# Performance work log

Hardware: AMD Instinct MI355X
Metric: run time of the kernel (lower is better)

## Reference

```python
import jax, jax.numpy as jnp
import numpy as np

HEAD_DIM = 128

def setup_inputs() -> dict:
    key = jax.random.key(0)
    k1, k2, k3 = jax.random.split(key, 3)
    B, Q, H, D = 1, 2048, 32, HEAD_DIM
    KV = 2048
    q = jax.random.normal(k1, (B, Q, H, D), dtype=jnp.float32)
    k = jax.random.normal(k2, (B, KV, H, D), dtype=jnp.float32)
    v = jax.random.normal(k3, (B, KV, H, D), dtype=jnp.float32)
    return {"q": q, "k": k, "v": v}

def reference(q, k, v):
    B, Q, H, D = q.shape
    KV = k.shape[1]
    scale = 1.0 / jnp.sqrt(jnp.asarray(D, dtype=q.dtype))
    # [B,H,Q,KV] scores
    scores = jnp.einsum('bqhd,bkhd->bhqk', q, k) * scale
    # causal mask: disallow j > i + (KV - Q)
    i = jnp.arange(Q)[:, None]
    j = jnp.arange(KV)[None, :]
    causal = j <= i + (KV - Q)  # [Q,KV]
    scores = jnp.where(causal[None, None], scores, -jnp.inf)
    probs = jax.nn.softmax(scores.astype(jnp.float32), axis=-1)
    out = jnp.einsum('bhqk,bkhd->bqhd', probs.astype(q.dtype), v)
    roco_score = probs.sum(axis=2)            # [B,H,KV]
    roco_sq_score = (probs ** 2).sum(axis=2)  # [B,H,KV]
    return out, roco_score, roco_sq_score
```

## Files before the change

kernel.cpp:

```cpp
#include <hip/hip_runtime.h>
#include <hip/hip_bf16.h>

typedef unsigned short u16;
typedef __attribute__((ext_vector_type(8))) short bf16x8;
typedef __attribute__((ext_vector_type(4))) float f32x4;

#define NH   32
#define HD   128
#define SEQ  2048
#define BQ   64
#define BK   64

#define VT_OFF 8192

__device__ __forceinline__ int vt_key(int d) { return (d & 7) ^ ((d >> 3) & 7); }

__device__ __forceinline__ u16 f2b(float x) {
  __hip_bfloat16 hb = __float2bfloat16(x);
  return *(u16*)&hb;
}

__device__ __forceinline__ bf16x8 cvt8(const float* src) {
  float4 a = *(const float4*)(src);
  float4 b = *(const float4*)(src + 4);
  u16 t[8];
  t[0] = f2b(a.x); t[1] = f2b(a.y); t[2] = f2b(a.z); t[3] = f2b(a.w);
  t[4] = f2b(b.x); t[5] = f2b(b.y); t[6] = f2b(b.z); t[7] = f2b(b.w);
  return *(bf16x8*)t;
}

__device__ __forceinline__ bf16x8 cvt8s(const float* src, float sc) {
  float4 a = *(const float4*)(src);
  float4 b = *(const float4*)(src + 4);
  u16 t[8];
  t[0] = f2b(a.x * sc); t[1] = f2b(a.y * sc); t[2] = f2b(a.z * sc); t[3] = f2b(a.w * sc);
  t[4] = f2b(b.x * sc); t[5] = f2b(b.y * sc); t[6] = f2b(b.z * sc); t[7] = f2b(b.w * sc);
  return *(bf16x8*)t;
}

__device__ __forceinline__ void dma16(const u16* g, u16* l) {
  __builtin_amdgcn_global_load_lds(
      (const __attribute__((address_space(1))) void*)g,
      (__attribute__((address_space(3))) void*)l, 16, 0, 0);
}

__global__ __launch_bounds__(256)
void prep(const float* __restrict__ K, const float* __restrict__ V,
          u16* __restrict__ Kb, u16* __restrict__ Vtb) {
  __shared__ __align__(16) u16 T[64 * 136];
  int b = (int)blockIdx.x;
  int tid = (int)threadIdx.x;
  if (b < 4096) {
    size_t i = (size_t)b * 256 + tid;
    bf16x8 v = cvt8(K + i * 8);
    *(uint4*)(Kb + i * 8) = *(uint4*)&v;
  } else {
    b -= 4096;
    int h = b >> 5, jt = b & 31;
    #pragma unroll
    for (int it = 0; it < 4; ++it) {
      int c = tid + it * 256;
      int j = c >> 4, grp = c & 15;
      bf16x8 v = cvt8(V + ((size_t)(jt * 64 + j) * NH + h) * HD + (grp << 3));
      *(uint4*)(T + j * 136 + ((grp ^ ((j >> 3) & 7)) << 3)) = *(uint4*)&v;
    }
    __syncthreads();
    #pragma unroll
    for (int it = 0; it < 2; ++it) {
      int c = tid + it * 256;
      int d0 = (c >> 3) << 1, k = c & 7, jg = k << 3;
      int off = (((d0 >> 3) ^ k) << 3) | (d0 & 7);
      u16 lo[8], hi[8];
      #pragma unroll
      for (int e = 0; e < 8; ++e) {
        unsigned w = *(const unsigned*)(T + (jg + e) * 136 + off);
        lo[e] = (u16)w; hi[e] = (u16)(w >> 16);
      }
      *(uint4*)(Vtb + ((size_t)h * HD + d0) * SEQ + jt * 64 + jg) = *(uint4*)lo;
      *(uint4*)(Vtb + ((size_t)h * HD + d0 + 1) * SEQ + jt * 64 + jg) = *(uint4*)hi;
    }
  }
}

template <bool PRE>
__global__ __launch_bounds__(256)
void attn_roco(const float* __restrict__ Qg, const float* __restrict__ Kg,
               const float* __restrict__ Vg, const u16* __restrict__ Kb,
               const u16* __restrict__ Vtb, float* __restrict__ Og,
               float* __restrict__ RS) {
  __shared__ __align__(16) u16 smem[16384];
  u16* Ks = smem;
  u16* Vt = smem + VT_OFF;
  u16* Ps = smem;

  const int tid = threadIdx.x;
  const int wv  = tid >> 6;
  const int ln  = tid & 63;
  const int qd  = ln >> 4;
  const int cc  = ln & 15;

  const int h = (int)blockIdx.x & 31;
  const int pos = ((int)blockIdx.x >> 5) & 7;
  const int grp = (int)blockIdx.x >> 8;
  int qt;
  if      (grp == 0) qt = 31 - pos;
  else if (grp == 1) qt = 16 + pos;
  else if (grp == 2) qt = 15 - pos;
  else               qt = pos;

  const int qbase  = qt * BQ;
  const int ntiles = qt + 1;

  const float qsc = 0.08838834764831845f * 1.4426950408889634f;
  bf16x8 qf[4];
  {
    const float* qp = Qg + ((size_t)(qbase + wv * 16 + cc) * NH + h) * HD;
    #pragma unroll
    for (int kd = 0; kd < 4; ++kd)
      qf[kd] = cvt8s(qp + kd * 32 + qd * 8, qsc);
  }

  const int rbase = wv * 16 + qd * 4;
  float ls[4] = {0.f, 0.f, 0.f, 0.f};

  if (PRE) {
    const int ntA = (qt >> 1) + 1;
    for (int ta = 0; ta < ntA; ++ta) {
      __syncthreads();
      #pragma unroll
      for (int it = 0; it < 8; ++it) {
        int c = it * 256 + tid;
        int row = c >> 4, g = (c & 15) ^ (row & 15);
        dma16(Kb + ((size_t)(ta * 128 + row) * NH + h) * HD + (g << 3),
              smem + (size_t)c * 8);
      }
      __syncthreads();

      f32x4 S[8];
      #pragma unroll
      for (int f = 0; f < 8; ++f)
        #pragma unroll
        for (int r = 0; r < 4; ++r) S[f][r] = 0.f;

      #pragma unroll
      for (int kd = 0; kd < 4; ++kd) {
        #pragma unroll
        for (int f = 0; f < 8; ++f) {
          bf16x8 b = *(const bf16x8*)(smem + (f * 16 + cc) * 128 +
                                      (((kd * 4 + qd) ^ cc) << 3));
          S[f] = __builtin_amdgcn_mfma_f32_16x16x32_bf16(qf[kd], b, S[f], 0, 0, 0);
        }
      }

      const bool last = (ta == ntA - 1);
      #pragma unroll
      for (int r = 0; r < 4; ++r) {
        const int ig = qbase + rbase + r;
        float acc = 0.f;
        #pragma unroll
        for (int f = 0; f < 8; ++f) {
          float e = __builtin_amdgcn_exp2f(S[f][r]);
          if (last && (ta * 128 + f * 16 + cc) > ig) e = 0.f;
          acc += e;
        }
        ls[r] += acc;
      }
    }
  } else {
    for (int t = 0; t < ntiles; ++t) {
      __syncthreads();
      #pragma unroll
      for (int it = 0; it < 4; ++it) {
        int c = tid + it * 256;
        int row = c >> 4, g = c & 15;
        bf16x8 kv = cvt8(Kg + ((size_t)(t * BK + row) * NH + h) * HD + (g << 3));
        *(uint4*)(Ks + row * 128 + ((g ^ (row & 15)) << 3)) = *(uint4*)&kv;
      }
      __syncthreads();

      f32x4 S[4];
      #pragma unroll
      for (int f = 0; f < 4; ++f)
        #pragma unroll
        for (int r = 0; r < 4; ++r) S[f][r] = 0.f;

      #pragma unroll
      for (int kd = 0; kd < 4; ++kd) {
        #pragma unroll
        for (int f = 0; f < 4; ++f) {
          bf16x8 b = *(const bf16x8*)(Ks + (f * 16 + cc) * 128 +
                                      (((kd * 4 + qd) ^ cc) << 3));
          S[f] = __builtin_amdgcn_mfma_f32_16x16x32_bf16(qf[kd], b, S[f], 0, 0, 0);
        }
      }

      const bool diag = (t == qt);
      #pragma unroll
      for (int r = 0; r < 4; ++r) {
        const int iloc = rbase + r;
        float acc = 0.f;
        #pragma unroll
        for (int f = 0; f < 4; ++f) {
          float e = __builtin_amdgcn_exp2f(S[f][r]);
          if (diag && (f * 16 + cc) > iloc) e = 0.f;
          acc += e;
        }
        ls[r] += acc;
      }
    }
  }

  float invl[4];
  #pragma unroll
  for (int r = 0; r < 4; ++r) {
    #pragma unroll
    for (int off = 1; off < 16; off <<= 1)
      ls[r] += __shfl_xor(ls[r], off);
    invl[r] = 1.f / ls[r];
  }

  f32x4 O[8];
  #pragma unroll
  for (int f = 0; f < 8; ++f)
    #pragma unroll
    for (int r = 0; r < 4; ++r) O[f][r] = 0.f;

  float* ws_s = RS + (size_t)h * SEQ;
  float* ws_q = RS + (size_t)NH * SEQ + (size_t)h * SEQ;

  for (int t = 0; t < ntiles; ++t) {
    __syncthreads();
    if (PRE) {
      #pragma unroll
      for (int it = 0; it < 4; ++it) {
        int c = it * 256 + tid;
        int row = c >> 4, g = (c & 15) ^ (row & 15);
        dma16(Kb + ((size_t)(t * BK + row) * NH + h) * HD + (g << 3),
              Ks + (size_t)c * 8);
      }
      #pragma unroll
      for (int it = 0; it < 4; ++it) {
        int c = it * 256 + tid;
        int d = c >> 3, g = (c & 7) ^ vt_key(d);
        dma16(Vtb + ((size_t)h * HD + d) * SEQ + t * BK + (g << 3),
              Vt + (size_t)c * 8);
      }
    } else {
      #pragma unroll
      for (int it = 0; it < 4; ++it) {
        int c = tid + it * 256;
        int row = c >> 4, g = c & 15;
        bf16x8 kv = cvt8(Kg + ((size_t)(t * BK + row) * NH + h) * HD + (g << 3));
        *(uint4*)(Ks + row * 128 + ((g ^ (row & 15)) << 3)) = *(uint4*)&kv;
      }
      #pragma unroll
      for (int it = 0; it < 4; ++it) {
        int c = tid + it * 256;
        int j = c >> 4, d0 = (c & 15) << 3;
        bf16x8 v = cvt8(Vg + ((size_t)(t * BK + j) * NH + h) * HD + d0);
        u16 ev[8];
        *(uint4*)ev = *(uint4*)&v;
        #pragma unroll
        for (int e = 0; e < 8; ++e) {
          int d = d0 + e;
          Vt[d * BK + ((((j >> 3) ^ vt_key(d)) << 3)) + (j & 7)] = ev[e];
        }
      }
    }
    __syncthreads();

    f32x4 S[4];
    #pragma unroll
    for (int f = 0; f < 4; ++f)
      #pragma unroll
      for (int r = 0; r < 4; ++r) S[f][r] = 0.f;

    #pragma unroll
    for (int kd = 0; kd < 4; ++kd) {
      #pragma unroll
      for (int f = 0; f < 4; ++f) {
        bf16x8 b = *(const bf16x8*)(Ks + (f * 16 + cc) * 128 +
                                    (((kd * 4 + qd) ^ cc) << 3));
        S[f] = __builtin_amdgcn_mfma_f32_16x16x32_bf16(qf[kd], b, S[f], 0, 0, 0);
      }
    }

    __syncthreads();

    const bool diag = (t == qt);
    float cs[4] = {0.f, 0.f, 0.f, 0.f}, cq[4] = {0.f, 0.f, 0.f, 0.f};
    #pragma unroll
    for (int r = 0; r < 4; ++r) {
      const int iloc = rbase + r;
      const int prow = wv * 16 + qd * 4 + r;
      #pragma unroll
      for (int f = 0; f < 4; ++f) {
        float p = __builtin_amdgcn_exp2f(S[f][r]) * invl[r];
        if (diag && (f * 16 + cc) > iloc) p = 0.f;
        cs[f] += p;
        cq[f] += p * p;
        int pg = f * 2 + (cc >> 3);
        Ps[prow * 64 + ((pg ^ (prow & 7)) << 3) + (cc & 7)] = f2b(p);
      }
    }
    #pragma unroll
    for (int f = 0; f < 4; ++f) {
      cs[f] += __shfl_xor(cs[f], 16); cs[f] += __shfl_xor(cs[f], 32);
      cq[f] += __shfl_xor(cq[f], 16); cq[f] += __shfl_xor(cq[f], 32);
      if (qd == f) {
        int j = t * BK + f * 16 + cc;
        atomicAdd(ws_s + j, cs[f]);
        atomicAdd(ws_q + j, cq[f]);
      }
    }
    #pragma unroll
    for (int ks2 = 0; ks2 < 2; ++ks2) {
      bf16x8 a = *(const bf16x8*)(Ps + (wv * 16 + cc) * 64 +
                                  (((ks2 * 4 + qd) ^ (cc & 7)) << 3));
      #pragma unroll
      for (int f2 = 0; f2 < 8; ++f2) {
        int d = f2 * 16 + cc;
        int jb = ks2 * 4 + qd;
        bf16x8 b = *(const bf16x8*)(Vt + d * BK + ((jb ^ vt_key(d)) << 3));
        O[f2] = __builtin_amdgcn_mfma_f32_16x16x32_bf16(a, b, O[f2], 0, 0, 0);
      }
    }
  }

  #pragma unroll
  for (int f2 = 0; f2 < 8; ++f2) {
    #pragma unroll
    for (int r = 0; r < 4; ++r) {
      int i = qbase + rbase + r;
      int d = f2 * 16 + cc;
      Og[((size_t)i * NH + h) * HD + d] = O[f2][r];
    }
  }
}

extern "C" void kernel_launch(void* const* d_in, const int* in_sizes, int n_in,
                              void* d_out, int out_size, void* d_ws, size_t ws_size,
                              hipStream_t stream) {
  (void)in_sizes; (void)n_in; (void)out_size;
  const float* Qg = (const float*)d_in[0];
  const float* Kg = (const float*)d_in[1];
  const float* Vg = (const float*)d_in[2];
  float* Og = (float*)d_out;

  const size_t roco_elems = (size_t)2 * NH * SEQ;
  const size_t tens = (size_t)SEQ * NH * HD;
  const size_t need = 2 * tens * 2;
  const bool pre = ws_size >= need;

  float* RS = Og + tens;
  (void)hipMemsetAsync(RS, 0, roco_elems * sizeof(float), stream);

  u16* Kb  = (u16*)d_ws;
  u16* Vtb = Kb + tens;

  if (pre) {
    prep<<<dim3(4096 + 1024), dim3(256), 0, stream>>>(Kg, Vg, Kb, Vtb);
    attn_roco<true><<<dim3(NH * (SEQ / BQ)), dim3(256), 0, stream>>>(
        Qg, Kg, Vg, Kb, Vtb, Og, RS);
  } else {
    attn_roco<false><<<dim3(NH * (SEQ / BQ)), dim3(256), 0, stream>>>(
        Qg, Kg, Vg, Kb, Vtb, Og, RS);
  }
}
```

Before: 239.1 us.

## Transpose denominator pass to split keys across waves and skip masked key rows

```diff
diff --git a/kernel.cpp b/kernel.cpp
--- a/kernel.cpp
+++ b/kernel.cpp
@@ -12,6 +12,7 @@
 #define BK   64
 
 #define VT_OFF 8192
+#define PS_OFF 16384
 
 __device__ __forceinline__ int vt_key(int d) { return (d & 7) ^ ((d >> 3) & 7); }
 
@@ -88,10 +89,10 @@
                const float* __restrict__ Vg, const u16* __restrict__ Kb,
                const u16* __restrict__ Vtb, float* __restrict__ Og,
                float* __restrict__ RS) {
-  __shared__ __align__(16) u16 smem[16384];
+  __shared__ __align__(16) u16 smem[20480];
   u16* Ks = smem;
   u16* Vt = smem + VT_OFF;
-  u16* Ps = smem;
+  u16* Ps = smem + PS_OFF;
 
   const int tid = threadIdx.x;
   const int wv  = tid >> 6;
@@ -121,10 +122,20 @@
   }
 
   const int rbase = wv * 16 + qd * 4;
-  float ls[4] = {0.f, 0.f, 0.f, 0.f};
+  float invl[4];
 
   if (PRE) {
     const int ntA = (qt >> 1) + 1;
+    bf16x8 qa[4][4];
+    #pragma unroll
+    for (int fq = 0; fq < 4; ++fq) {
+      const float* qp = Qg + ((size_t)(qbase + fq * 16 + cc) * NH + h) * HD;
+      #pragma unroll
+      for (int kd = 0; kd < 4; ++kd)
+        qa[fq][kd] = cvt8s(qp + kd * 32 + qd * 8, qsc);
+    }
+    float lsw[4] = {0.f, 0.f, 0.f, 0.f};
+
     for (int ta = 0; ta < ntA; ++ta) {
       __syncthreads();
       #pragma unroll
@@ -136,37 +147,65 @@
       }
       __syncthreads();
 
-      f32x4 S[8];
-      #pragma unroll
-      for (int f = 0; f < 8; ++f)
-        #pragma unroll
-        for (int r = 0; r < 4; ++r) S[f][r] = 0.f;
-
-      #pragma unroll
-      for (int kd = 0; kd < 4; ++kd) {
-        #pragma unroll
-        for (int f = 0; f < 8; ++f) {
-          bf16x8 b = *(const bf16x8*)(smem + (f * 16 + cc) * 128 +
-                                      (((kd * 4 + qd) ^ cc) << 3));
-          S[f] = __builtin_amdgcn_mfma_f32_16x16x32_bf16(qf[kd], b, S[f], 0, 0, 0);
+      const bool last = (ta == ntA - 1);
+      const int rem = qbase + 64 - ta * 128;
+      if (!last || wv * 32 < rem) {
+        f32x4 S0[4], S1[4];
+        #pragma unroll
+        for (int fq = 0; fq < 4; ++fq)
+          #pragma unroll
+          for (int r = 0; r < 4; ++r) { S0[fq][r] = 0.f; S1[fq][r] = 0.f; }
+
+        #pragma unroll
+        for (int kd = 0; kd < 4; ++kd) {
+          bf16x8 a0 = *(const bf16x8*)(smem + (wv * 32 + cc) * 128 +
+                                       (((kd * 4 + qd) ^ cc) << 3));
+          bf16x8 a1 = *(const bf16x8*)(smem + (wv * 32 + 16 + cc) * 128 +
+                                       (((kd * 4 + qd) ^ cc) << 3));
+          #pragma unroll
+          for (int fq = 0; fq < 4; ++fq) {
+            S0[fq] = __builtin_amdgcn_mfma_f32_16x16x32_bf16(a0, qa[fq][kd], S0[fq], 0, 0, 0);
+            S1[fq] = __builtin_amdgcn_mfma_f32_16x16x32_bf16(a1, qa[fq][kd], S1[fq], 0, 0, 0);
+          }
         }
-      }
-
-      const bool last = (ta == ntA - 1);
-      #pragma unroll
-      for (int r = 0; r < 4; ++r) {
-        const int ig = qbase + rbase + r;
-        float acc = 0.f;
-        #pragma unroll
-        for (int f = 0; f < 8; ++f) {
-          float e = __builtin_amdgcn_exp2f(S[f][r]);
-          if (last && (ta * 128 + f * 16 + cc) > ig) e = 0.f;
-          acc += e;
+
+        const int kb = ta * 128 + wv * 32 + qd * 4;
+        #pragma unroll
+        for (int fq = 0; fq < 4; ++fq) {
+          const int qg = qbase + fq * 16 + cc;
+          float acc = 0.f;
+          #pragma unroll
+          for (int r = 0; r < 4; ++r) {
+            float e0 = __builtin_amdgcn_exp2f(S0[fq][r]);
+            float e1 = __builtin_amdgcn_exp2f(S1[fq][r]);
+            if (last && (kb + r) > qg) e0 = 0.f;
+            if (last && (kb + 16 + r) > qg) e1 = 0.f;
+            acc += e0 + e1;
+          }
+          lsw[fq] += acc;
         }
-        ls[r] += acc;
-      }
+      }
+    }
+    #pragma unroll
+    for (int fq = 0; fq < 4; ++fq) {
+      lsw[fq] += __shfl_xor(lsw[fq], 16);
+      lsw[fq] += __shfl_xor(lsw[fq], 32);
+    }
+    float* ls_lds = (float*)(smem + PS_OFF);
+    if (ln < 16) {
+      #pragma unroll
+      for (int fq = 0; fq < 4; ++fq)
+        ls_lds[wv * 64 + fq * 16 + ln] = lsw[fq];
+    }
+    __syncthreads();
+    #pragma unroll
+    for (int r = 0; r < 4; ++r) {
+      const int q = rbase + r;
+      invl[r] = 1.f / (ls_lds[q] + ls_lds[64 + q] +
+                       ls_lds[128 + q] + ls_lds[192 + q]);
     }
   } else {
+    float ls[4] = {0.f, 0.f, 0.f, 0.f};
     for (int t = 0; t < ntiles; ++t) {
       __syncthreads();
       #pragma unroll
@@ -208,15 +247,13 @@
         ls[r] += acc;
       }
     }
-  }
-
-  float invl[4];
-  #pragma unroll
-  for (int r = 0; r < 4; ++r) {
-    #pragma unroll
-    for (int off = 1; off < 16; off <<= 1)
-      ls[r] += __shfl_xor(ls[r], off);
-    invl[r] = 1.f / ls[r];
+    #pragma unroll
+    for (int r = 0; r < 4; ++r) {
+      #pragma unroll
+      for (int off = 1; off < 16; off <<= 1)
+        ls[r] += __shfl_xor(ls[r], off);
+      invl[r] = 1.f / ls[r];
+    }
   }
 
   f32x4 O[8];
@@ -284,8 +321,6 @@
         S[f] = __builtin_amdgcn_mfma_f32_16x16x32_bf16(qf[kd], b, S[f], 0, 0, 0);
       }
     }
-
-    __syncthreads();
 
     const bool diag = (t == qt);
     float cs[4] = {0.f, 0.f, 0.f, 0.f}, cq[4] = {0.f, 0.f, 0.f, 0.f};
```

Result: slower. 309.4 us (+29.4%).
